# Optimization experiments

Hardware: AMD Instinct MI355X
Metric: run time of the kernel (lower is better)

The kernel has to match this reference:

```python
import jax, jax.numpy as jnp
import numpy as np

N = 100000      # nodes
E = 1600000     # edges (avg degree 16)
IN, HID, OUT = 128, 128, 64


def setup_inputs() -> dict:
    key = jax.random.key(0)
    k1, k2, k3, k4 = jax.random.split(key, 4)
    x = jax.random.normal(k1, (N, IN), dtype=jnp.float32)
    edge_index = jax.random.randint(k2, (2, E), 0, N, dtype=jnp.int64)
    # GCNConv linear weights (glorot-ish scale) and zero biases
    W1 = jax.random.normal(k3, (IN, HID), dtype=jnp.float32) * (1.0 / np.sqrt(IN))
    b1 = jnp.zeros((HID,), jnp.float32)
    W2 = jax.random.normal(k4, (HID, OUT), dtype=jnp.float32) * (1.0 / np.sqrt(HID))
    b2 = jnp.zeros((OUT,), jnp.float32)
    return {"x": x, "edge_index": edge_index, "W1": W1, "b1": b1, "W2": W2, "b2": b2}


def reference(x, edge_index, W1, b1, W2, b2):
    n = x.shape[0]
    loops = jnp.arange(n, dtype=edge_index.dtype)
    self_e = jnp.stack([loops, loops])  # [2, N]
    # forward() explicitly adds self-loops, then PyG GCNConv's gcn_norm
    # (add_self_loops=True by default) adds a second set -> duplicate (i,i) edges.
    ei = jnp.concatenate([edge_index, self_e, self_e], axis=1)
    row, col = ei[0], ei[1]  # source, target

    # symmetric normalization: deg over target index, norm_e = d^-1/2[row]*d^-1/2[col]
    deg = jax.ops.segment_sum(jnp.ones(row.shape, x.dtype), col, num_segments=n)
    dis = jax.lax.rsqrt(deg)  # deg >= 2 thanks to self-loops
    norm = dis[row] * dis[col]  # [E']

    def gcn_conv(h, W, b):
        h = h @ W                               # transform first (PyG order)
        msg = h[row] * norm[:, None]            # gather + per-edge scale
        agg = jax.ops.segment_sum(msg, col, num_segments=n)  # scatter-add
        return agg + b

    h = jax.nn.relu(gcn_conv(x, W1, b1))
    return gcn_conv(h, W2, b2)
```

## Files before the change

### kernel.cpp

```cpp
#include <hip/hip_runtime.h>
#include <hip/hip_fp16.h>

#define NPB   512
#define NBMAX 256
#define CHUNK 4096

using f16x4 = __attribute__((ext_vector_type(4))) _Float16;
using f32x4 = __attribute__((ext_vector_type(4))) float;

__global__ void k_detect(const int* __restrict__ ei32, int* __restrict__ flag,
                         int* __restrict__ bcnt, int nb) {
  int t = threadIdx.x;
  if (t < nb) bcnt[t] = 0;
  if (t == 0) {
    int z = 1;
    for (int k = 0; k < 64; ++k)
      if (ei32[2 * k + 1] != 0) { z = 0; break; }
    flag[0] = z;
  }
}

__device__ __forceinline__ int edge_at(const void* ei, int is64, long long pos) {
  return is64 ? (int)((const long long*)ei)[pos] : ((const int*)ei)[pos];
}

__global__ __launch_bounds__(256) void k_bcount(const void* __restrict__ ei,
                                                const int* __restrict__ flag,
                                                int E, int* __restrict__ bcnt, int nb) {
  __shared__ int cnt[NBMAX];
  int t = threadIdx.x;
  cnt[t] = 0;
  __syncthreads();
  int is64 = flag[0];
  int stride = gridDim.x * blockDim.x;
  for (int e = blockIdx.x * blockDim.x + t; e < E; e += stride) {
    int c = edge_at(ei, is64, (long long)E + e);
    atomicAdd(&cnt[c >> 9], 1);
  }
  __syncthreads();
  if (t < nb && cnt[t]) atomicAdd(&bcnt[t], cnt[t]);
}

__global__ void k_bscan(const int* __restrict__ bcnt, int* __restrict__ bbase,
                        int* __restrict__ bcur, int* __restrict__ rowptr,
                        int nb, int N, int E) {
  __shared__ int sh[NBMAX];
  int t = threadIdx.x;
  sh[t] = (t < nb) ? bcnt[t] : 0;
  __syncthreads();
  for (int off = 1; off < NBMAX; off <<= 1) {
    int x = 0;
    if (t >= off) x = sh[t - off];
    __syncthreads();
    if (t >= off) sh[t] += x;
    __syncthreads();
  }
  int excl = t ? sh[t - 1] : 0;
  if (t < nb) { bbase[t] = excl; bcur[t] = excl; }
  if (t == 0) { bbase[nb] = E; rowptr[N] = E; }
}

__global__ __launch_bounds__(256) void k_fillB(const void* __restrict__ ei,
                                               const int* __restrict__ flag, int E,
                                               int* __restrict__ bcur,
                                               int* __restrict__ tmp, int nb) {
  __shared__ int cntL[NBMAX], startL[NBMAX], curL[NBMAX], gofs[NBMAX];
  __shared__ int sh[NBMAX];
  __shared__ int stage[CHUNK];
  __shared__ unsigned char sbkt[CHUNK];
  int t = threadIdx.x;
  int is64 = flag[0];
  for (long long base = (long long)blockIdx.x * CHUNK; base < E;
       base += (long long)gridDim.x * CHUNK) {
    int m = (int)min((long long)CHUNK, (long long)E - base);
    cntL[t] = 0;
    __syncthreads();
    for (int i = t; i < m; i += 256) {
      int c = edge_at(ei, is64, (long long)E + base + i);
      atomicAdd(&cntL[c >> 9], 1);
    }
    __syncthreads();
    sh[t] = cntL[t];
    __syncthreads();
    for (int off = 1; off < NBMAX; off <<= 1) {
      int x = 0;
      if (t >= off) x = sh[t - off];
      __syncthreads();
      if (t >= off) sh[t] += x;
      __syncthreads();
    }
    int excl = t ? sh[t - 1] : 0;
    startL[t] = excl;
    curL[t] = excl;
    if (t < nb && cntL[t] > 0) gofs[t] = atomicAdd(&bcur[t], cntL[t]);
    __syncthreads();
    for (int i = t; i < m; i += 256) {
      int r = edge_at(ei, is64, base + i);
      int c = edge_at(ei, is64, (long long)E + base + i);
      int b = c >> 9;
      int p = atomicAdd(&curL[b], 1);
      stage[p] = ((c & 511) << 17) | r;
      sbkt[p] = (unsigned char)b;
    }
    __syncthreads();
    for (int i = t; i < m; i += 256) {
      int b = sbkt[i];
      tmp[gofs[b] + (i - startL[b])] = stage[i];
    }
    __syncthreads();
  }
}

__global__ __launch_bounds__(256) void k_fillC(const int* __restrict__ tmp,
                                               const int* __restrict__ bbase,
                                               int* __restrict__ rowptr,
                                               float* __restrict__ dis,
                                               int* __restrict__ esrc, int N) {
  __shared__ int cnt[NPB];
  __shared__ int loc[NPB];
  __shared__ int sh[256];
  int b = blockIdx.x, t = threadIdx.x;
  int beg = bbase[b], end = bbase[b + 1];
  int base_node = b << 9;
  cnt[t] = 0; cnt[t + 256] = 0;
  __syncthreads();
  for (int e = beg + t; e < end; e += 256)
    atomicAdd(&cnt[tmp[e] >> 17], 1);
  __syncthreads();
  int c0 = cnt[2 * t], c1 = cnt[2 * t + 1];
  sh[t] = c0 + c1;
  __syncthreads();
  for (int off = 1; off < 256; off <<= 1) {
    int x = 0;
    if (t >= off) x = sh[t - off];
    __syncthreads();
    if (t >= off) sh[t] += x;
    __syncthreads();
  }
  int pre = t ? sh[t - 1] : 0;
  loc[2 * t] = beg + pre;
  loc[2 * t + 1] = beg + pre + c0;
  int v0 = base_node + 2 * t, v1 = v0 + 1;
  if (v0 < N) { rowptr[v0] = beg + pre;      dis[v0] = rsqrtf((float)(c0 + 2)); }
  if (v1 < N) { rowptr[v1] = beg + pre + c0; dis[v1] = rsqrtf((float)(c1 + 2)); }
  __syncthreads();
  for (int e = beg + t; e < end; e += 256) {
    int u = tmp[e];
    int pos = atomicAdd(&loc[u >> 17], 1);
    esrc[pos] = u & 0x1FFFF;
  }
}

template <int BN, bool AHALF>
__global__ __launch_bounds__(256) void k_gemm_mfma(const void* __restrict__ Av,
                                                   const float* __restrict__ W,
                                                   __half* __restrict__ C,
                                                   int M, int tiles) {
  __shared__ _Float16 Wt[BN][136];
  __shared__ _Float16 At[64][136];
  constexpr int NT = BN / 64;
  constexpr int CH = BN / 4;
  int t = threadIdx.x;
  int lane = t & 63, w = t >> 6;
  int lrow = lane & 15;
  int kq = (lane >> 4) * 4;
  int wcol0 = w * (BN / 4);

  for (int idx = t; idx < 128 * BN / 4; idx += 256) {
    int k = idx / CH, c4 = (idx % CH) * 4;
    float4 v = *(const float4*)&W[(size_t)k * BN + c4];
    Wt[c4 + 0][k] = (_Float16)v.x;
    Wt[c4 + 1][k] = (_Float16)v.y;
    Wt[c4 + 2][k] = (_Float16)v.z;
    Wt[c4 + 3][k] = (_Float16)v.w;
  }

  for (int tile = blockIdx.x; tile < tiles; tile += gridDim.x) {
    int row0 = tile * 64;
    __syncthreads();
#pragma unroll
    for (int i = 0; i < 8; ++i) {
      int idx = t + i * 256;
      int r = idx >> 5, c = (idx & 31) * 4;
      int gr = row0 + r;
      f16x4 hv = {0, 0, 0, 0};
      if (gr < M) {
        if constexpr (AHALF) {
          hv = *(const f16x4*)&((const _Float16*)Av)[(size_t)gr * 128 + c];
        } else {
          float4 v = *(const float4*)&((const float*)Av)[(size_t)gr * 128 + c];
          hv = f16x4{(_Float16)v.x, (_Float16)v.y, (_Float16)v.z, (_Float16)v.w};
        }
      }
      *(f16x4*)&At[r][c] = hv;
    }
    __syncthreads();
    f32x4 acc[4][NT];
#pragma unroll
    for (int mt = 0; mt < 4; ++mt)
#pragma unroll
      for (int nt = 0; nt < NT; ++nt) acc[mt][nt] = f32x4{0.f, 0.f, 0.f, 0.f};
#pragma unroll
    for (int k0 = 0; k0 < 128; k0 += 16) {
      int kk = k0 + kq;
      f16x4 a[4], b[NT];
#pragma unroll
      for (int mt = 0; mt < 4; ++mt)
        a[mt] = *(const f16x4*)&At[mt * 16 + lrow][kk];
#pragma unroll
      for (int nt = 0; nt < NT; ++nt)
        b[nt] = *(const f16x4*)&Wt[wcol0 + nt * 16 + lrow][kk];
#pragma unroll
      for (int mt = 0; mt < 4; ++mt)
#pragma unroll
        for (int nt = 0; nt < NT; ++nt)
          acc[mt][nt] = __builtin_amdgcn_mfma_f32_16x16x16f16(a[mt], b[nt],
                                                              acc[mt][nt], 0, 0, 0);
    }
    __syncthreads();
#pragma unroll
    for (int mt = 0; mt < 4; ++mt)
#pragma unroll
      for (int nt = 0; nt < NT; ++nt) {
        int cc = wcol0 + nt * 16 + lrow;
        int rr = mt * 16 + kq;
#pragma unroll
        for (int reg = 0; reg < 4; ++reg)
          At[rr + reg][cc] = (_Float16)acc[mt][nt][reg];
      }
    __syncthreads();
#pragma unroll
    for (int i = 0; i < BN / 16; ++i) {
      int idx = t + i * 256;
      int r = idx / CH, c = (idx % CH) * 4;
      int gr = row0 + r;
      if (gr < M)
        *(f16x4*)&C[(size_t)gr * BN + c] = *(const f16x4*)&At[r][c];
    }
  }
}

__global__ __launch_bounds__(256) void k_gather128(const __half* __restrict__ t,
    const float* __restrict__ bias, const int* __restrict__ rowptr,
    const int* __restrict__ esrc, const float* __restrict__ dis,
    __half* __restrict__ o, int n) {
  int gw = (int)((blockIdx.x * blockDim.x + threadIdx.x) >> 6);
  int lane = threadIdx.x & 63;
  int nw = (int)((gridDim.x * blockDim.x) >> 6);
  int half = lane >> 5;
  int f = (lane & 31) * 4;
  for (int v = gw; v < n; v += nw) {
    float dv = dis[v];
    float a0 = 0.f, a1 = 0.f, a2 = 0.f, a3 = 0.f;
    int beg = rowptr[v], end = rowptr[v + 1];
    int e = beg + half;
    for (; e + 6 < end; e += 8) {
      int s0 = esrc[e], s1 = esrc[e + 2], s2 = esrc[e + 4], s3 = esrc[e + 6];
      float n0 = dis[s0] * dv, n1 = dis[s1] * dv;
      float n2 = dis[s2] * dv, n3 = dis[s3] * dv;
      uint2 u0 = *(const uint2*)&t[(size_t)s0 * 128 + f];
      uint2 u1 = *(const uint2*)&t[(size_t)s1 * 128 + f];
      uint2 u2 = *(const uint2*)&t[(size_t)s2 * 128 + f];
      uint2 u3 = *(const uint2*)&t[(size_t)s3 * 128 + f];
      __half2 p;
      p = *(__half2*)&u0.x; a0 = fmaf(n0, __low2float(p), a0); a1 = fmaf(n0, __high2float(p), a1);
      p = *(__half2*)&u0.y; a2 = fmaf(n0, __low2float(p), a2); a3 = fmaf(n0, __high2float(p), a3);
      p = *(__half2*)&u1.x; a0 = fmaf(n1, __low2float(p), a0); a1 = fmaf(n1, __high2float(p), a1);
      p = *(__half2*)&u1.y; a2 = fmaf(n1, __low2float(p), a2); a3 = fmaf(n1, __high2float(p), a3);
      p = *(__half2*)&u2.x; a0 = fmaf(n2, __low2float(p), a0); a1 = fmaf(n2, __high2float(p), a1);
      p = *(__half2*)&u2.y; a2 = fmaf(n2, __low2float(p), a2); a3 = fmaf(n2, __high2float(p), a3);
      p = *(__half2*)&u3.x; a0 = fmaf(n3, __low2float(p), a0); a1 = fmaf(n3, __high2float(p), a1);
      p = *(__half2*)&u3.y; a2 = fmaf(n3, __low2float(p), a2); a3 = fmaf(n3, __high2float(p), a3);
    }
    for (; e < end; e += 2) {
      int s0 = esrc[e];
      float n0 = dis[s0] * dv;
      uint2 u0 = *(const uint2*)&t[(size_t)s0 * 128 + f];
      __half2 p;
      p = *(__half2*)&u0.x; a0 = fmaf(n0, __low2float(p), a0); a1 = fmaf(n0, __high2float(p), a1);
      p = *(__half2*)&u0.y; a2 = fmaf(n0, __low2float(p), a2); a3 = fmaf(n0, __high2float(p), a3);
    }
    if (half == 0) {
      float s = 2.f * dv * dv;
      uint2 uv = *(const uint2*)&t[(size_t)v * 128 + f];
      __half2 p;
      p = *(__half2*)&uv.x; a0 = fmaf(s, __low2float(p), a0); a1 = fmaf(s, __high2float(p), a1);
      p = *(__half2*)&uv.y; a2 = fmaf(s, __low2float(p), a2); a3 = fmaf(s, __high2float(p), a3);
    }
    a0 += __shfl_xor(a0, 32); a1 += __shfl_xor(a1, 32);
    a2 += __shfl_xor(a2, 32); a3 += __shfl_xor(a3, 32);
    if (half == 0) {
      a0 = fmaxf(a0 + bias[f], 0.f);
      a1 = fmaxf(a1 + bias[f + 1], 0.f);
      a2 = fmaxf(a2 + bias[f + 2], 0.f);
      a3 = fmaxf(a3 + bias[f + 3], 0.f);
      __half2 h0 = __floats2half2_rn(a0, a1), h1 = __floats2half2_rn(a2, a3);
      uint2 uu;
      uu.x = *(unsigned int*)&h0; uu.y = *(unsigned int*)&h1;
      *(uint2*)&o[(size_t)v * 128 + f] = uu;
    }
  }
}

__global__ __launch_bounds__(256) void k_gather64(const __half* __restrict__ t,
    const float* __restrict__ bias, const int* __restrict__ rowptr,
    const int* __restrict__ esrc, const float* __restrict__ dis,
    float* __restrict__ o, int n) {
  int gw = (int)((blockIdx.x * blockDim.x + threadIdx.x) >> 6);
  int lane = threadIdx.x & 63;
  int nw = (int)((gridDim.x * blockDim.x) >> 6);
  int sub = lane >> 4;
  int f = (lane & 15) * 4;
  for (int v = gw; v < n; v += nw) {
    float dv = dis[v];
    float a0 = 0.f, a1 = 0.f, a2 = 0.f, a3 = 0.f;
    int beg = rowptr[v], end = rowptr[v + 1];
    int e = beg + sub;
    for (; e + 7 < end; e += 8) {
      int s0 = esrc[e], s1 = esrc[e + 4];
      float n0 = dis[s0] * dv, n1 = dis[s1] * dv;
      uint2 u0 = *(const uint2*)&t[(size_t)s0 * 64 + f];
      uint2 u1 = *(const uint2*)&t[(size_t)s1 * 64 + f];
      __half2 p;
      p = *(__half2*)&u0.x; a0 = fmaf(n0, __low2float(p), a0); a1 = fmaf(n0, __high2float(p), a1);
      p = *(__half2*)&u0.y; a2 = fmaf(n0, __low2float(p), a2); a3 = fmaf(n0, __high2float(p), a3);
      p = *(__half2*)&u1.x; a0 = fmaf(n1, __low2float(p), a0); a1 = fmaf(n1, __high2float(p), a1);
      p = *(__half2*)&u1.y; a2 = fmaf(n1, __low2float(p), a2); a3 = fmaf(n1, __high2float(p), a3);
    }
    for (; e < end; e += 4) {
      int s0 = esrc[e];
      float n0 = dis[s0] * dv;
      uint2 u0 = *(const uint2*)&t[(size_t)s0 * 64 + f];
      __half2 p;
      p = *(__half2*)&u0.x; a0 = fmaf(n0, __low2float(p), a0); a1 = fmaf(n0, __high2float(p), a1);
      p = *(__half2*)&u0.y; a2 = fmaf(n0, __low2float(p), a2); a3 = fmaf(n0, __high2float(p), a3);
    }
    if (sub == 0) {
      float s = 2.f * dv * dv;
      uint2 uv = *(const uint2*)&t[(size_t)v * 64 + f];
      __half2 p;
      p = *(__half2*)&uv.x; a0 = fmaf(s, __low2float(p), a0); a1 = fmaf(s, __high2float(p), a1);
      p = *(__half2*)&uv.y; a2 = fmaf(s, __low2float(p), a2); a3 = fmaf(s, __high2float(p), a3);
    }
    a0 += __shfl_xor(a0, 16); a0 += __shfl_xor(a0, 32);
    a1 += __shfl_xor(a1, 16); a1 += __shfl_xor(a1, 32);
    a2 += __shfl_xor(a2, 16); a2 += __shfl_xor(a2, 32);
    a3 += __shfl_xor(a3, 16); a3 += __shfl_xor(a3, 32);
    if (sub == 0) {
      float4 r;
      r.x = a0 + bias[f];     r.y = a1 + bias[f + 1];
      r.z = a2 + bias[f + 2]; r.w = a3 + bias[f + 3];
      *(float4*)&o[(size_t)v * 64 + f] = r;
    }
  }
}

extern "C" void kernel_launch(void* const* d_in, const int* in_sizes, int n_in,
                              void* d_out, int out_size, void* d_ws, size_t ws_size,
                              hipStream_t stream) {
  const float* x  = (const float*)d_in[0];
  const void*  ei = d_in[1];
  const float* W1 = (const float*)d_in[2];
  const float* b1 = (const float*)d_in[3];
  const float* W2 = (const float*)d_in[4];
  const float* b2 = (const float*)d_in[5];
  const int N = in_sizes[0] / 128;
  const int E = in_sizes[1] / 2;
  float* out = (float*)d_out;
  const int nb = (N + NPB - 1) / NPB;

  size_t off = 0;
  auto alloc = [&](size_t bytes) -> void* {
    void* p = (char*)d_ws + off;
    off += (bytes + 255) & ~(size_t)255;
    return p;
  };
  int*    flag   = (int*)alloc(4);
  int*    bcnt   = (int*)alloc(NBMAX * 4);
  int*    bbase  = (int*)alloc((NBMAX + 1) * 4);
  int*    bcur   = (int*)alloc(NBMAX * 4);
  int*    rowptr = (int*)alloc(((size_t)N + 1) * 4);
  float*  dis    = (float*)alloc((size_t)N * 4);
  int*    tmp    = (int*)alloc((size_t)E * 4);
  int*    esrc   = (int*)alloc((size_t)E * 4);
  __half* t1     = (__half*)alloc((size_t)N * 128 * 2);
  __half* z1     = (__half*)alloc((size_t)N * 128 * 2);
  __half* t2     = t1;

  int nchunks = (E + CHUNK - 1) / CHUNK;
  int tiles = (N + 63) / 64;

  k_detect<<<1, 256, 0, stream>>>((const int*)ei, flag, bcnt, nb);
  k_bcount<<<1024, 256, 0, stream>>>(ei, flag, E, bcnt, nb);
  k_bscan<<<1, 256, 0, stream>>>(bcnt, bbase, bcur, rowptr, nb, N, E);
  k_fillB<<<nchunks, 256, 0, stream>>>(ei, flag, E, bcur, tmp, nb);
  k_fillC<<<nb, 256, 0, stream>>>(tmp, bbase, rowptr, dis, esrc, N);

  k_gemm_mfma<128, false><<<min(tiles, 768), 256, 0, stream>>>(x, W1, t1, N, tiles);
  k_gather128<<<2048, 256, 0, stream>>>(t1, b1, rowptr, esrc, dis, z1, N);
  k_gemm_mfma<64, true><<<min(tiles, 768), 256, 0, stream>>>(z1, W2, t2, N, tiles);
  k_gather64<<<2048, 256, 0, stream>>>(t2, b2, rowptr, esrc, dis, out, N);
}
```

Before: 241.1 us.

## Fold source-side degree normalization into GEMM epilogue and deepen gather unrolling

The GEMM epilogue now scales each output row by dis[row], so the gathers no longer load dis[src] for every edge. Instead they sum the pre-scaled features and multiply by dis[v] once at the end. The self-loop term becomes 2*t[v]. The gather loops are also unrolled wider (16 edges per iteration) for more memory-level parallelism, and CHUNK for the edge fill is halved. This removes one random dis load and multiply per edge. In exchange it adds an fp16 rounding step on the scaled values and higher register pressure.

```diff
diff --git a/kernel.cpp b/kernel.cpp
--- a/kernel.cpp
+++ b/kernel.cpp
@@ -3,7 +3,7 @@
 
 #define NPB   512
 #define NBMAX 256
-#define CHUNK 4096
+#define CHUNK 2048
 
 using f16x4 = __attribute__((ext_vector_type(4))) _Float16;
 using f32x4 = __attribute__((ext_vector_type(4))) float;
@@ -154,10 +154,12 @@
 template <int BN, bool AHALF>
 __global__ __launch_bounds__(256) void k_gemm_mfma(const void* __restrict__ Av,
                                                    const float* __restrict__ W,
+                                                   const float* __restrict__ dis,
                                                    __half* __restrict__ C,
                                                    int M, int tiles) {
   __shared__ _Float16 Wt[BN][136];
   __shared__ _Float16 At[64][136];
+  __shared__ float disL[64];
   constexpr int NT = BN / 64;
   constexpr int CH = BN / 4;
   int t = threadIdx.x;
@@ -194,6 +196,10 @@
       }
       *(f16x4*)&At[r][c] = hv;
     }
+    if (t < 64) {
+      int gr = row0 + t;
+      disL[t] = (gr < M) ? dis[gr] : 0.f;
+    }
     __syncthreads();
     f32x4 acc[4][NT];
 #pragma unroll
@@ -226,7 +232,7 @@
         int rr = mt * 16 + kq;
 #pragma unroll
         for (int reg = 0; reg < 4; ++reg)
-          At[rr + reg][cc] = (_Float16)acc[mt][nt][reg];
+          At[rr + reg][cc] = (_Float16)(acc[mt][nt][reg] * disL[rr + reg]);
       }
     __syncthreads();
 #pragma unroll
@@ -239,6 +245,11 @@
     }
   }
 }
+
+#define ACC4(u)                                                         \
+  { __half2 p;                                                          \
+    p = *(__half2*)&(u).x; a0 += __low2float(p); a1 += __high2float(p); \
+    p = *(__half2*)&(u).y; a2 += __low2float(p); a3 += __high2float(p); }
 
 __global__ __launch_bounds__(256) void k_gather128(const __half* __restrict__ t,
     const float* __restrict__ bias, const int* __restrict__ rowptr,
@@ -250,50 +261,50 @@
   int half = lane >> 5;
   int f = (lane & 31) * 4;
   for (int v = gw; v < n; v += nw) {
-    float dv = dis[v];
     float a0 = 0.f, a1 = 0.f, a2 = 0.f, a3 = 0.f;
     int beg = rowptr[v], end = rowptr[v + 1];
     int e = beg + half;
-    for (; e + 6 < end; e += 8) {
-      int s0 = esrc[e], s1 = esrc[e + 2], s2 = esrc[e + 4], s3 = esrc[e + 6];
-      float n0 = dis[s0] * dv, n1 = dis[s1] * dv;
-      float n2 = dis[s2] * dv, n3 = dis[s3] * dv;
+    for (; e + 14 < end; e += 16) {
+      int s0 = esrc[e],      s1 = esrc[e + 2],  s2 = esrc[e + 4],  s3 = esrc[e + 6];
+      int s4 = esrc[e + 8],  s5 = esrc[e + 10], s6 = esrc[e + 12], s7 = esrc[e + 14];
       uint2 u0 = *(const uint2*)&t[(size_t)s0 * 128 + f];
       uint2 u1 = *(const uint2*)&t[(size_t)s1 * 128 + f];
       uint2 u2 = *(const uint2*)&t[(size_t)s2 * 128 + f];
       uint2 u3 = *(const uint2*)&t[(size_t)s3 * 128 + f];
-      __half2 p;
-      p = *(__half2*)&u0.x; a0 = fmaf(n0, __low2float(p), a0); a1 = fmaf(n0, __high2float(p), a1);
-      p = *(__half2*)&u0.y; a2 = fmaf(n0, __low2float(p), a2); a3 = fmaf(n0, __high2float(p), a3);
-      p = *(__half2*)&u1.x; a0 = fmaf(n1, __low2float(p), a0); a1 = fmaf(n1, __high2float(p), a1);
-      p = *(__half2*)&u1.y; a2 = fmaf(n1, __low2float(p), a2); a3 = fmaf(n1, __high2float(p), a3);
-      p = *(__half2*)&u2.x; a0 = fmaf(n2, __low2float(p), a0); a1 = fmaf(n2, __high2float(p), a1);
-      p = *(__half2*)&u2.y; a2 = fmaf(n2, __low2float(p), a2); a3 = fmaf(n2, __high2float(p), a3);
-      p = *(__half2*)&u3.x; a0 = fmaf(n3, __low2float(p), a0); a1 = fmaf(n3, __high2float(p), a1);
-      p = *(__half2*)&u3.y; a2 = fmaf(n3, __low2float(p), a2); a3 = fmaf(n3, __high2float(p), a3);
+      uint2 u4 = *(const uint2*)&t[(size_t)s4 * 128 + f];
+      uint2 u5 = *(const uint2*)&t[(size_t)s5 * 128 + f];
+      uint2 u6 = *(const uint2*)&t[(size_t)s6 * 128 + f];
+      uint2 u7 = *(const uint2*)&t[(size_t)s7 * 128 + f];
+      ACC4(u0) ACC4(u1) ACC4(u2) ACC4(u3)
+      ACC4(u4) ACC4(u5) ACC4(u6) ACC4(u7)
+    }
+    for (; e + 6 < end; e += 8) {
+      int s0 = esrc[e], s1 = esrc[e + 2], s2 = esrc[e + 4], s3 = esrc[e + 6];
+      uint2 u0 = *(const uint2*)&t[(size_t)s0 * 128 + f];
+      uint2 u1 = *(const uint2*)&t[(size_t)s1 * 128 + f];
+      uint2 u2 = *(const uint2*)&t[(size_t)s2 * 128 + f];
+      uint2 u3 = *(const uint2*)&t[(size_t)s3 * 128 + f];
+      ACC4(u0) ACC4(u1) ACC4(u2) ACC4(u3)
     }
     for (; e < end; e += 2) {
       int s0 = esrc[e];
-      float n0 = dis[s0] * dv;
       uint2 u0 = *(const uint2*)&t[(size_t)s0 * 128 + f];
-      __half2 p;
-      p = *(__half2*)&u0.x; a0 = fmaf(n0, __low2float(p), a0); a1 = fmaf(n0, __high2float(p), a1);
-      p = *(__half2*)&u0.y; a2 = fmaf(n0, __low2float(p), a2); a3 = fmaf(n0, __high2float(p), a3);
+      ACC4(u0)
     }
     if (half == 0) {
-      float s = 2.f * dv * dv;
       uint2 uv = *(const uint2*)&t[(size_t)v * 128 + f];
       __half2 p;
-      p = *(__half2*)&uv.x; a0 = fmaf(s, __low2float(p), a0); a1 = fmaf(s, __high2float(p), a1);
-      p = *(__half2*)&uv.y; a2 = fmaf(s, __low2float(p), a2); a3 = fmaf(s, __high2float(p), a3);
+      p = *(__half2*)&uv.x; a0 = fmaf(2.f, __low2float(p), a0); a1 = fmaf(2.f, __high2float(p), a1);
+      p = *(__half2*)&uv.y; a2 = fmaf(2.f, __low2float(p), a2); a3 = fmaf(2.f, __high2float(p), a3);
     }
     a0 += __shfl_xor(a0, 32); a1 += __shfl_xor(a1, 32);
     a2 += __shfl_xor(a2, 32); a3 += __shfl_xor(a3, 32);
     if (half == 0) {
-      a0 = fmaxf(a0 + bias[f], 0.f);
-      a1 = fmaxf(a1 + bias[f + 1], 0.f);
-      a2 = fmaxf(a2 + bias[f + 2], 0.f);
-      a3 = fmaxf(a3 + bias[f + 3], 0.f);
+      float dv = dis[v];
+      a0 = fmaxf(fmaf(dv, a0, bias[f]),     0.f);
+      a1 = fmaxf(fmaf(dv, a1, bias[f + 1]), 0.f);
+      a2 = fmaxf(fmaf(dv, a2, bias[f + 2]), 0.f);
+      a3 = fmaxf(fmaf(dv, a3, bias[f + 3]), 0.f);
       __half2 h0 = __floats2half2_rn(a0, a1), h1 = __floats2half2_rn(a2, a3);
       uint2 uu;
       uu.x = *(unsigned int*)&h0; uu.y = *(unsigned int*)&h1;
@@ -312,44 +323,37 @@
   int sub = lane >> 4;
   int f = (lane & 15) * 4;
   for (int v = gw; v < n; v += nw) {
-    float dv = dis[v];
     float a0 = 0.f, a1 = 0.f, a2 = 0.f, a3 = 0.f;
     int beg = rowptr[v], end = rowptr[v + 1];
     int e = beg + sub;
-    for (; e + 7 < end; e += 8) {
-      int s0 = esrc[e], s1 = esrc[e + 4];
-      float n0 = dis[s0] * dv, n1 = dis[s1] * dv;
+    for (; e + 12 < end; e += 16) {
+      int s0 = esrc[e], s1 = esrc[e + 4], s2 = esrc[e + 8], s3 = esrc[e + 12];
       uint2 u0 = *(const uint2*)&t[(size_t)s0 * 64 + f];
       uint2 u1 = *(const uint2*)&t[(size_t)s1 * 64 + f];
-      __half2 p;
-      p = *(__half2*)&u0.x; a0 = fmaf(n0, __low2float(p), a0); a1 = fmaf(n0, __high2float(p), a1);
-      p = *(__half2*)&u0.y; a2 = fmaf(n0, __low2float(p), a2); a3 = fmaf(n0, __high2float(p), a3);
-      p = *(__half2*)&u1.x; a0 = fmaf(n1, __low2float(p), a0); a1 = fmaf(n1, __high2float(p), a1);
-      p = *(__half2*)&u1.y; a2 = fmaf(n1, __low2float(p), a2); a3 = fmaf(n1, __high2float(p), a3);
+      uint2 u2 = *(const uint2*)&t[(size_t)s2 * 64 + f];
+      uint2 u3 = *(const uint2*)&t[(size_t)s3 * 64 + f];
+      ACC4(u0) ACC4(u1) ACC4(u2) ACC4(u3)
     }
     for (; e < end; e += 4) {
       int s0 = esrc[e];
-      float n0 = dis[s0] * dv;
       uint2 u0 = *(const uint2*)&t[(size_t)s0 * 64 + f];
-      __half2 p;
-      p = *(__half2*)&u0.x; a0 = fmaf(n0, __low2float(p), a0); a1 = fmaf(n0, __high2float(p), a1);
-      p = *(__half2*)&u0.y; a2 = fmaf(n0, __low2float(p), a2); a3 = fmaf(n0, __high2float(p), a3);
+      ACC4(u0)
     }
     if (sub == 0) {
-      float s = 2.f * dv * dv;
       uint2 uv = *(const uint2*)&t[(size_t)v * 64 + f];
       __half2 p;
-      p = *(__half2*)&uv.x; a0 = fmaf(s, __low2float(p), a0); a1 = fmaf(s, __high2float(p), a1);
-      p = *(__half2*)&uv.y; a2 = fmaf(s, __low2float(p), a2); a3 = fmaf(s, __high2float(p), a3);
+      p = *(__half2*)&uv.x; a0 = fmaf(2.f, __low2float(p), a0); a1 = fmaf(2.f, __high2float(p), a1);
+      p = *(__half2*)&uv.y; a2 = fmaf(2.f, __low2float(p), a2); a3 = fmaf(2.f, __high2float(p), a3);
     }
     a0 += __shfl_xor(a0, 16); a0 += __shfl_xor(a0, 32);
     a1 += __shfl_xor(a1, 16); a1 += __shfl_xor(a1, 32);
     a2 += __shfl_xor(a2, 16); a2 += __shfl_xor(a2, 32);
     a3 += __shfl_xor(a3, 16); a3 += __shfl_xor(a3, 32);
     if (sub == 0) {
+      float dv = dis[v];
       float4 r;
-      r.x = a0 + bias[f];     r.y = a1 + bias[f + 1];
-      r.z = a2 + bias[f + 2]; r.w = a3 + bias[f + 3];
+      r.x = fmaf(dv, a0, bias[f]);     r.y = fmaf(dv, a1, bias[f + 1]);
+      r.z = fmaf(dv, a2, bias[f + 2]); r.w = fmaf(dv, a3, bias[f + 3]);
       *(float4*)&o[(size_t)v * 64 + f] = r;
     }
   }
@@ -396,8 +400,8 @@
   k_fillB<<<nchunks, 256, 0, stream>>>(ei, flag, E, bcur, tmp, nb);
   k_fillC<<<nb, 256, 0, stream>>>(tmp, bbase, rowptr, dis, esrc, N);
 
-  k_gemm_mfma<128, false><<<min(tiles, 768), 256, 0, stream>>>(x, W1, t1, N, tiles);
+  k_gemm_mfma<128, false><<<min(tiles, 768), 256, 0, stream>>>(x, W1, dis, t1, N, tiles);
   k_gather128<<<2048, 256, 0, stream>>>(t1, b1, rowptr, esrc, dis, z1, N);
-  k_gemm_mfma<64, true><<<min(tiles, 768), 256, 0, stream>>>(z1, W2, t2, N, tiles);
+  k_gemm_mfma<64, true><<<min(tiles, 768), 256, 0, stream>>>(z1, W2, dis, t2, N, tiles);
   k_gather64<<<2048, 256, 0, stream>>>(t2, b2, rowptr, esrc, dis, out, N);
 }
```

Measured after the change: 241.7 us. About the same (+0.2%).
